# Kernel optimization log

Hardware: AMD Instinct MI355X
Metric: run time of the kernel (lower is better)

## Reference

```python
import jax, jax.numpy as jnp
import numpy as np

B, C, H, W = 8, 256, 64, 64
CI = C // 2  # inter_channels


def setup_inputs() -> dict:
    key = jax.random.key(0)
    ks = jax.random.split(key, 9)
    s_in = 1.0 / np.sqrt(C)
    s_ci = 1.0 / np.sqrt(CI)
    return {
        "x": jax.random.normal(ks[0], (B, C, H, W), dtype=jnp.float32),
        "g_w": jax.random.uniform(ks[1], (CI, C), jnp.float32, -s_in, s_in),
        "g_b": jax.random.uniform(ks[2], (CI,), jnp.float32, -s_in, s_in),
        "theta_w": jax.random.uniform(ks[3], (CI, C), jnp.float32, -s_in, s_in),
        "theta_b": jax.random.uniform(ks[4], (CI,), jnp.float32, -s_in, s_in),
        "phi_w": jax.random.uniform(ks[5], (CI, C), jnp.float32, -s_in, s_in),
        "phi_b": jax.random.uniform(ks[6], (CI,), jnp.float32, -s_in, s_in),
        "W_w": jax.random.uniform(ks[7], (C, CI), jnp.float32, -s_ci, s_ci),
        "W_b": jax.random.uniform(ks[8], (C,), jnp.float32, -s_ci, s_ci),
    }


def reference(x, g_w, g_b, theta_w, theta_b, phi_w, phi_b, W_w, W_b):
    b, c, h, w = x.shape
    xf = x.reshape(b, c, h * w)  # [B, C, N]
    # 1x1 convs == per-pixel linear maps
    g_x = jnp.einsum("oc,bcn->bon", g_w, xf) + g_b[:, None]      # [B, CI, N]
    theta_x = jnp.einsum("oc,bcn->bon", theta_w, xf) + theta_b[:, None]
    phi_x = jnp.einsum("oc,bcn->bon", phi_w, xf) + phi_b[:, None]
    # attention_map[b, i, j] = <theta[:, i], phi[:, j]>, softmax over j
    attn = jax.nn.softmax(jnp.einsum("bci,bcj->bij", theta_x, phi_x), axis=-1)
    # y[b, c, i] = sum_j g_x[b, c, j] * attn[b, i, j]
    y = jnp.einsum("bcj,bij->bci", g_x, attn)  # [B, CI, N]
    out = jnp.einsum("oc,bcn->bon", W_w, y) + W_b[:, None]  # [B, C, N]
    return out.reshape(b, c, h, w) + x
```

## Files before the change

### kernel.cpp

```cpp
#include <hip/hip_runtime.h>
#include <hip/hip_bf16.h>

#define B_  8
#define C_  256
#define CI_ 128
#define N_  4096

typedef __bf16 bf16;
typedef __attribute__((ext_vector_type(8))) __bf16 bf16x8;
typedef __attribute__((ext_vector_type(4))) __bf16 bf16x4;
typedef __attribute__((ext_vector_type(4))) float  floatx4;

static_assert(sizeof(bf16) == 2, "bf16 size");

__device__ inline floatx4 mfma16(bf16x8 a, bf16x8 b, floatx4 c) {
    return __builtin_amdgcn_mfma_f32_16x16x32_bf16(a, b, c, 0, 0, 0);
}

__device__ inline bool detect_fp32(const void* probe) {
    const unsigned short* u = (const unsigned short*)probe;
    int lane = threadIdx.x & 63;
    unsigned short w = u[lane * 2];
    int ex = (w >> 7) & 0xFF;
    bool insane = !((ex > 96 && ex < 143) || (w & 0x7FFF) == 0);
    unsigned long long b = __ballot(insane);
    return __popcll(b) > 16;
}

__device__ inline bf16x8 load8(const void* p, size_t i, bool fp32) {
    if (!fp32) return *(const bf16x8*)((const bf16*)p + i);
    const float* f = (const float*)p + i;
    floatx4 a = *(const floatx4*)(f);
    floatx4 c = *(const floatx4*)(f + 4);
    bf16x8 r;
    r[0] = (bf16)a[0]; r[1] = (bf16)a[1]; r[2] = (bf16)a[2]; r[3] = (bf16)a[3];
    r[4] = (bf16)c[0]; r[5] = (bf16)c[1]; r[6] = (bf16)c[2]; r[7] = (bf16)c[3];
    return r;
}

__device__ inline float loadv(const void* p, size_t i, bool fp32) {
    return fp32 ? ((const float*)p)[i] : (float)((const bf16*)p)[i];
}

__global__ __launch_bounds__(256) void proj_kernel(
    const void* __restrict__ x,
    const void* __restrict__ wt, const void* __restrict__ bt,
    const void* __restrict__ wp, const void* __restrict__ bp,
    const void* __restrict__ wg, const void* __restrict__ bg,
    bf16* __restrict__ T, bf16* __restrict__ P, bf16* __restrict__ G)
{
    const bool fp32 = detect_fp32(x);

    const int b    = blockIdx.y;
    const int n0   = blockIdx.x * 128;
    const int proj = blockIdx.z;

    const void* w    = (proj == 0) ? wt : (proj == 1) ? wp : wg;
    const void* bias = (proj == 0) ? bt : (proj == 1) ? bp : bg;

    __shared__ bf16 xT[128][40];

    const int t    = threadIdx.x;
    const int wid  = t >> 6;
    const int lane = t & 63;
    const int l15  = lane & 15;
    const int quad = lane >> 4;
    const int wm   = wid >> 1;
    const int wn   = wid & 1;

    floatx4 acc[4][4];
#pragma unroll
    for (int i = 0; i < 4; ++i)
#pragma unroll
        for (int j = 0; j < 4; ++j) acc[i][j] = (floatx4)0.f;

    const int cl  = t & 31;
    const int pxg = (t >> 5) * 8;

    const int obase_w = ((proj == 2) ? wm : wn) * 64;
    const int pbase_x = ((proj == 2) ? wn : wm) * 64;

    for (int k = 0; k < C_; k += 32) {
#pragma unroll
        for (int half = 0; half < 2; ++half) {
            int px = pxg + half * 64;
            bf16x8 v = load8(x, ((size_t)b * C_ + k + cl) * N_ + n0 + px, fp32);
#pragma unroll
            for (int i = 0; i < 8; ++i) xT[px + i][cl] = v[i];
        }
        __syncthreads();

        bf16x8 fw[4], fx[4];
#pragma unroll
        for (int i = 0; i < 4; ++i) {
            int o  = obase_w + i * 16 + l15;
            fw[i] = load8(w, (size_t)o * C_ + k + quad * 8, fp32);
            int px = pbase_x + i * 16 + l15;
            fx[i] = *(const bf16x8*)(&xT[px][quad * 8]);
        }
        if (proj == 2) {
#pragma unroll
            for (int mi = 0; mi < 4; ++mi)
#pragma unroll
                for (int ni = 0; ni < 4; ++ni)
                    acc[mi][ni] = mfma16(fw[mi], fx[ni], acc[mi][ni]);
        } else {
#pragma unroll
            for (int mi = 0; mi < 4; ++mi)
#pragma unroll
                for (int ni = 0; ni < 4; ++ni)
                    acc[mi][ni] = mfma16(fx[mi], fw[ni], acc[mi][ni]);
        }
        __syncthreads();
    }

    if (proj < 2) {
        bf16* out = ((proj == 0) ? T : P) + (size_t)b * N_ * CI_;
#pragma unroll
        for (int mi = 0; mi < 4; ++mi)
#pragma unroll
            for (int ni = 0; ni < 4; ++ni)
#pragma unroll
                for (int r = 0; r < 4; ++r) {
                    int px = n0 + wm * 64 + mi * 16 + quad * 4 + r;
                    int o  = wn * 64 + ni * 16 + l15;
                    out[(size_t)px * CI_ + o] =
                        (bf16)(acc[mi][ni][r] + loadv(bias, o, fp32));
                }
    } else {
        bf16* out = G + (size_t)b * CI_ * N_;
#pragma unroll
        for (int mi = 0; mi < 4; ++mi)
#pragma unroll
            for (int ni = 0; ni < 4; ++ni)
#pragma unroll
                for (int r = 0; r < 4; ++r) {
                    int o  = wm * 64 + mi * 16 + quad * 4 + r;
                    int px = n0 + wn * 64 + ni * 16 + l15;
                    out[(size_t)o * N_ + px] =
                        (bf16)(acc[mi][ni][r] + loadv(bias, o, fp32));
                }
    }
}

__global__ __launch_bounds__(512) void attn_kernel(
    const bf16* __restrict__ T,
    const bf16* __restrict__ P,
    const bf16* __restrict__ G,
    const void* __restrict__ Ww,
    const void* __restrict__ Wb,
    const void* __restrict__ x,
    void* __restrict__ out)
{
    const int bid = blockIdx.x;
    const int b   = bid & 7;
    const int i0  = (bid >> 3) * 128;

    __shared__ __align__(16) char smem[143360];

    const bool fp32 = detect_fp32(x);

    const int t    = threadIdx.x;
    const int w    = t >> 6;
    const int g    = w >> 2;
    const int wg   = w & 3;
    const int tg   = t & 255;
    const int lane = t & 63;
    const int l15  = lane & 15;
    const int quad = lane >> 4;

    bf16* Kl = (bf16*)(smem + g * 35840);
    bf16* Vt = (bf16*)(smem + g * 35840 + 17408);
    bf16* Pw = (bf16*)(smem + 71680 + w * 4608);

    const bf16* Kb = P + (size_t)b * N_ * CI_;
    const bf16* Vb = G + (size_t)b * CI_ * N_;
    const int jbase = g * 2048;

    bf16x8 qf[2][4];
#pragma unroll
    for (int rf = 0; rf < 2; ++rf) {
        const bf16* Qb = T + ((size_t)b * N_ + i0 + wg * 32 + rf * 16 + l15) * CI_;
#pragma unroll
        for (int ks = 0; ks < 4; ++ks)
            qf[rf][ks] = *(const bf16x8*)(Qb + ks * 32 + quad * 8);
    }

    floatx4 O[2][8];
#pragma unroll
    for (int rf = 0; rf < 2; ++rf)
#pragma unroll
        for (int cf = 0; cf < 8; ++cf) O[rf][cf] = (floatx4)0.f;
    float lsum[2][4];
#pragma unroll
    for (int rf = 0; rf < 2; ++rf)
#pragma unroll
        for (int r = 0; r < 4; ++r) lsum[rf][r] = 0.f;

    bf16x8 kreg[4], vreg[4];
#pragma unroll
    for (int s = 0; s < 4; ++s) {
        int id = tg + s * 256;
        kreg[s] = *(const bf16x8*)(Kb + (size_t)(jbase + (id >> 4)) * CI_ + (id & 15) * 8);
        vreg[s] = *(const bf16x8*)(Vb + (size_t)(id >> 3) * N_ + jbase + (id & 7) * 8);
    }

    for (int it = 0; it < 32; ++it) {
#pragma unroll
        for (int s = 0; s < 4; ++s) {
            int id = tg + s * 256;
            *(bf16x8*)(Kl + (id >> 4) * 136 + (id & 15) * 8) = kreg[s];
            *(bf16x8*)(Vt + (id >> 3) * 72 + (id & 7) * 8) = vreg[s];
        }
        __syncthreads();

        if (it < 31) {
            int j0n = jbase + (it + 1) * 64;
#pragma unroll
            for (int s = 0; s < 4; ++s) {
                int id = tg + s * 256;
                kreg[s] = *(const bf16x8*)(Kb + (size_t)(j0n + (id >> 4)) * CI_ + (id & 15) * 8);
                vreg[s] = *(const bf16x8*)(Vb + (size_t)(id >> 3) * N_ + j0n + (id & 7) * 8);
            }
        }

        floatx4 S[2][4];
#pragma unroll
        for (int jf = 0; jf < 4; ++jf) {
            floatx4 s0 = (floatx4)0.f, s1 = (floatx4)0.f;
#pragma unroll
            for (int ks = 0; ks < 4; ++ks) {
                bf16x8 kf = *(const bf16x8*)(Kl + (jf * 16 + l15) * 136 + ks * 32 + quad * 8);
                s0 = mfma16(qf[0][ks], kf, s0);
                s1 = mfma16(qf[1][ks], kf, s1);
            }
            S[0][jf] = s0;
            S[1][jf] = s1;
        }

#pragma unroll
        for (int rf = 0; rf < 2; ++rf)
#pragma unroll
            for (int r = 0; r < 4; ++r) {
                float p0 = __expf(S[rf][0][r]);
                float p1 = __expf(S[rf][1][r]);
                float p2 = __expf(S[rf][2][r]);
                float p3 = __expf(S[rf][3][r]);
                lsum[rf][r] += (p0 + p1) + (p2 + p3);
                int row = rf * 16 + quad * 4 + r;
                Pw[row * 72 + 0 * 16 + l15] = (bf16)p0;
                Pw[row * 72 + 1 * 16 + l15] = (bf16)p1;
                Pw[row * 72 + 2 * 16 + l15] = (bf16)p2;
                Pw[row * 72 + 3 * 16 + l15] = (bf16)p3;
            }

#pragma unroll
        for (int ks = 0; ks < 2; ++ks) {
            bf16x8 pf0 = *(const bf16x8*)(Pw + l15 * 72 + ks * 32 + quad * 8);
            bf16x8 pf1 = *(const bf16x8*)(Pw + (16 + l15) * 72 + ks * 32 + quad * 8);
#pragma unroll
            for (int cf = 0; cf < 8; ++cf) {
                bf16x8 vf = *(const bf16x8*)(Vt + (cf * 16 + l15) * 72 + ks * 32 + quad * 8);
                O[0][cf] = mfma16(pf0, vf, O[0][cf]);
                O[1][cf] = mfma16(pf1, vf, O[1][cf]);
            }
        }
        __syncthreads();
    }

    float* scrO = (float*)smem;
    float* scrL = (float*)(smem + 71680);
    bf16*  Yl   = (bf16*)(smem + 108544);
    if (g == 1) {
#pragma unroll
        for (int rf = 0; rf < 2; ++rf)
#pragma unroll
            for (int cf = 0; cf < 8; ++cf)
#pragma unroll
                for (int r = 0; r < 4; ++r)
                    scrO[(rf * 32 + cf * 4 + r) * 256 + wg * 64 + lane] = O[rf][cf][r];
#pragma unroll
        for (int rf = 0; rf < 2; ++rf)
#pragma unroll
            for (int r = 0; r < 4; ++r)
                scrL[(rf * 4 + r) * 256 + wg * 64 + lane] = lsum[rf][r];
    }
    __syncthreads();
    if (g == 0) {
#pragma unroll
        for (int rf = 0; rf < 2; ++rf)
#pragma unroll
            for (int cf = 0; cf < 8; ++cf)
#pragma unroll
                for (int r = 0; r < 4; ++r)
                    O[rf][cf][r] += scrO[(rf * 32 + cf * 4 + r) * 256 + wg * 64 + lane];

#pragma unroll
        for (int rf = 0; rf < 2; ++rf)
#pragma unroll
            for (int r = 0; r < 4; ++r) {
                float rs = lsum[rf][r] + scrL[(rf * 4 + r) * 256 + wg * 64 + lane];
                rs += __shfl_xor(rs, 1);
                rs += __shfl_xor(rs, 2);
                rs += __shfl_xor(rs, 4);
                rs += __shfl_xor(rs, 8);
                lsum[rf][r] = 1.f / rs;
            }

#pragma unroll
        for (int rf = 0; rf < 2; ++rf)
#pragma unroll
            for (int cf = 0; cf < 8; ++cf)
#pragma unroll
                for (int r = 0; r < 4; ++r) {
                    int px = wg * 32 + rf * 16 + quad * 4 + r;
                    Yl[px * 136 + cf * 16 + l15] =
                        (bf16)(O[rf][cf][r] * lsum[rf][r]);
                }
    }
    __syncthreads();

    bf16* Wl = (bf16*)smem;
#pragma unroll
    for (int p = 0; p < 16; ++p) {
        int idx = p * 2048 + t * 4;
        int o   = idx >> 7;
        int ci  = idx & 127;
        bf16x4 v;
        if (fp32) {
            floatx4 f4 = *(const floatx4*)((const float*)Ww + idx);
            v[0] = (bf16)f4[0]; v[1] = (bf16)f4[1];
            v[2] = (bf16)f4[2]; v[3] = (bf16)f4[3];
        } else {
            v = *(const bf16x4*)((const bf16*)Ww + idx);
        }
        *(bf16x4*)(&Wl[o * 136 + ci]) = v;
    }
    __syncthreads();

    {
        const int wm = w >> 1;
        const int wn = w & 1;
        floatx4 acc[4][4];
#pragma unroll
        for (int i = 0; i < 4; ++i)
#pragma unroll
            for (int j = 0; j < 4; ++j) acc[i][j] = (floatx4)0.f;

#pragma unroll
        for (int ks = 0; ks < 4; ++ks) {
            bf16x8 fa[4], fb[4];
#pragma unroll
            for (int i = 0; i < 4; ++i) {
                fa[i] = *(const bf16x8*)(&Wl[(wm * 64 + i * 16 + l15) * 136 + ks * 32 + quad * 8]);
                fb[i] = *(const bf16x8*)(&Yl[(wn * 64 + i * 16 + l15) * 136 + ks * 32 + quad * 8]);
            }
#pragma unroll
            for (int mi = 0; mi < 4; ++mi)
#pragma unroll
                for (int ni = 0; ni < 4; ++ni)
                    acc[mi][ni] = mfma16(fa[mi], fb[ni], acc[mi][ni]);
        }

#pragma unroll
        for (int mi = 0; mi < 4; ++mi)
#pragma unroll
            for (int ni = 0; ni < 4; ++ni)
#pragma unroll
                for (int r = 0; r < 4; ++r) {
                    int oo = wm * 64 + mi * 16 + quad * 4 + r;
                    int px = i0 + wn * 64 + ni * 16 + l15;
                    size_t idx = ((size_t)b * C_ + oo) * N_ + px;
                    float v = acc[mi][ni][r] + loadv(Wb, oo, fp32)
                            + loadv(x, idx, fp32);
                    if (fp32) ((float*)out)[idx] = v;
                    else      ((bf16*)out)[idx] = (bf16)v;
                }
    }
}

extern "C" void kernel_launch(void* const* d_in, const int* in_sizes, int n_in,
                              void* d_out, int out_size, void* d_ws, size_t ws_size,
                              hipStream_t stream) {
    const void* x    = d_in[0];
    const void* g_w  = d_in[1];
    const void* g_b  = d_in[2];
    const void* th_w = d_in[3];
    const void* th_b = d_in[4];
    const void* ph_w = d_in[5];
    const void* ph_b = d_in[6];
    const void* W_w  = d_in[7];
    const void* W_b  = d_in[8];

    const size_t plane = (size_t)B_ * N_ * CI_;
    bf16* T = (bf16*)d_ws;
    bf16* P = T + plane;
    bf16* G = P + plane;

    proj_kernel<<<dim3(N_ / 128, B_, 3), 256, 0, stream>>>(
        x, th_w, th_b, ph_w, ph_b, g_w, g_b, T, P, G);
    attn_kernel<<<dim3(N_ / 128 * B_), 512, 0, stream>>>(
        T, P, G, W_w, W_b, x, d_out);
}
```

Baseline: 263.5 us.

## Fuse three projections into one kernel sharing the x tile, with prefetch

```diff
diff --git a/kernel.cpp b/kernel.cpp
--- a/kernel.cpp
+++ b/kernel.cpp
@@ -42,7 +42,14 @@
     return fp32 ? ((const float*)p)[i] : (float)((const bf16*)p)[i];
 }
 
-__global__ __launch_bounds__(256) void proj_kernel(
+__device__ inline bf16x8 cvt8(floatx4 a, floatx4 b) {
+    bf16x8 r;
+    r[0] = (bf16)a[0]; r[1] = (bf16)a[1]; r[2] = (bf16)a[2]; r[3] = (bf16)a[3];
+    r[4] = (bf16)b[0]; r[5] = (bf16)b[1]; r[6] = (bf16)b[2]; r[7] = (bf16)b[3];
+    return r;
+}
+
+__global__ __launch_bounds__(512) void proj3_kernel(
     const void* __restrict__ x,
     const void* __restrict__ wt, const void* __restrict__ bt,
     const void* __restrict__ wp, const void* __restrict__ bp,
@@ -51,95 +58,127 @@
 {
     const bool fp32 = detect_fp32(x);
 
-    const int b    = blockIdx.y;
-    const int n0   = blockIdx.x * 128;
-    const int proj = blockIdx.z;
-
-    const void* w    = (proj == 0) ? wt : (proj == 1) ? wp : wg;
-    const void* bias = (proj == 0) ? bt : (proj == 1) ? bp : bg;
+    const int b  = blockIdx.y;
+    const int n0 = blockIdx.x * 128;
 
     __shared__ bf16 xT[128][40];
+    __shared__ bf16 wl[384][40];
 
     const int t    = threadIdx.x;
-    const int wid  = t >> 6;
+    const int w    = t >> 6;
     const int lane = t & 63;
     const int l15  = lane & 15;
     const int quad = lane >> 4;
-    const int wm   = wid >> 1;
-    const int wn   = wid & 1;
-
-    floatx4 acc[4][4];
-#pragma unroll
-    for (int i = 0; i < 4; ++i)
-#pragma unroll
-        for (int j = 0; j < 4; ++j) acc[i][j] = (floatx4)0.f;
-
-    const int cl  = t & 31;
-    const int pxg = (t >> 5) * 8;
-
-    const int obase_w = ((proj == 2) ? wm : wn) * 64;
-    const int pbase_x = ((proj == 2) ? wn : wm) * 64;
-
-    for (int k = 0; k < C_; k += 32) {
-#pragma unroll
-        for (int half = 0; half < 2; ++half) {
-            int px = pxg + half * 64;
-            bf16x8 v = load8(x, ((size_t)b * C_ + k + cl) * N_ + n0 + px, fp32);
-#pragma unroll
-            for (int i = 0; i < 8; ++i) xT[px + i][cl] = v[i];
+    const int wm   = w >> 1;
+    const int wn   = w & 1;
+
+    const int sc = t >> 4;
+    const int sm = t & 15;
+    const int wr = t >> 2;
+    const int wc = (t & 3) * 8;
+
+    floatx4 acc[6][4];
+#pragma unroll
+    for (int f = 0; f < 6; ++f)
+#pragma unroll
+        for (int ni = 0; ni < 4; ++ni) acc[f][ni] = (floatx4)0.f;
+
+    floatx4 pxa, pxb; bf16x8 pxh;
+    floatx4 pwa[3], pwb[3]; bf16x8 pwh[3];
+
+    auto issue = [&](int k) {
+        size_t xo = ((size_t)b * C_ + k + sc) * N_ + n0 + sm * 8;
+        if (fp32) {
+            const float* fx_ = (const float*)x + xo;
+            pxa = *(const floatx4*)fx_;
+            pxb = *(const floatx4*)(fx_ + 4);
+        } else {
+            pxh = *(const bf16x8*)((const bf16*)x + xo);
+        }
+#pragma unroll
+        for (int p = 0; p < 3; ++p) {
+            const void* ws = (p == 0) ? wt : (p == 1) ? wp : wg;
+            size_t wo = (size_t)wr * C_ + k + wc;
+            if (fp32) {
+                const float* fw_ = (const float*)ws + wo;
+                pwa[p] = *(const floatx4*)fw_;
+                pwb[p] = *(const floatx4*)(fw_ + 4);
+            } else {
+                pwh[p] = *(const bf16x8*)((const bf16*)ws + wo);
+            }
+        }
+    };
+
+    issue(0);
+
+    for (int ks = 0; ks < 8; ++ks) {
+        {
+            bf16x8 xv = fp32 ? cvt8(pxa, pxb) : pxh;
+            int colx = ((((sc >> 3) + sm) & 3) << 3) + (sc & 7);
+#pragma unroll
+            for (int i = 0; i < 8; ++i) xT[sm * 8 + i][colx] = xv[i];
+#pragma unroll
+            for (int p = 0; p < 3; ++p) {
+                bf16x8 wv = fp32 ? cvt8(pwa[p], pwb[p]) : pwh[p];
+                *(bf16x8*)(&wl[p * 128 + wr][wc]) = wv;
+            }
         }
         __syncthreads();
 
-        bf16x8 fw[4], fx[4];
-#pragma unroll
-        for (int i = 0; i < 4; ++i) {
-            int o  = obase_w + i * 16 + l15;
-            fw[i] = load8(w, (size_t)o * C_ + k + quad * 8, fp32);
-            int px = pbase_x + i * 16 + l15;
-            fx[i] = *(const bf16x8*)(&xT[px][quad * 8]);
-        }
-        if (proj == 2) {
-#pragma unroll
-            for (int mi = 0; mi < 4; ++mi)
-#pragma unroll
-                for (int ni = 0; ni < 4; ++ni)
-                    acc[mi][ni] = mfma16(fw[mi], fx[ni], acc[mi][ni]);
+        if (ks < 7) issue((ks + 1) * 32);
+
+        bf16x8 fxr[4], fwr[6];
+#pragma unroll
+        for (int ni = 0; ni < 4; ++ni) {
+            int px = wn * 64 + ni * 16 + l15;
+            int ch = (quad + (px >> 3)) & 3;
+            fxr[ni] = *(const bf16x8*)(&xT[px][ch * 8]);
+        }
+#pragma unroll
+        for (int f = 0; f < 6; ++f)
+            fwr[f] = *(const bf16x8*)(&wl[f * 64 + wm * 16 + l15][quad * 8]);
+
+#pragma unroll
+        for (int f = 0; f < 4; ++f)
+#pragma unroll
+            for (int ni = 0; ni < 4; ++ni)
+                acc[f][ni] = mfma16(fxr[ni], fwr[f], acc[f][ni]);
+#pragma unroll
+        for (int f = 4; f < 6; ++f)
+#pragma unroll
+            for (int ni = 0; ni < 4; ++ni)
+                acc[f][ni] = mfma16(fwr[f], fxr[ni], acc[f][ni]);
+
+        __syncthreads();
+    }
+
+#pragma unroll
+    for (int f = 0; f < 6; ++f) {
+        const void* bsel = (f < 2) ? bt : (f < 4) ? bp : bg;
+        if (f < 4) {
+            bf16* outp = ((f < 2) ? T : P) + (size_t)b * N_ * CI_;
+            int o = (f & 1) * 64 + wm * 16 + l15;
+            float bv = loadv(bsel, o, fp32);
+#pragma unroll
+            for (int ni = 0; ni < 4; ++ni)
+#pragma unroll
+                for (int r = 0; r < 4; ++r) {
+                    int px = n0 + wn * 64 + ni * 16 + quad * 4 + r;
+                    outp[(size_t)px * CI_ + o] = (bf16)(acc[f][ni][r] + bv);
+                }
         } else {
-#pragma unroll
-            for (int mi = 0; mi < 4; ++mi)
-#pragma unroll
-                for (int ni = 0; ni < 4; ++ni)
-                    acc[mi][ni] = mfma16(fx[mi], fw[ni], acc[mi][ni]);
-        }
-        __syncthreads();
-    }
-
-    if (proj < 2) {
-        bf16* out = ((proj == 0) ? T : P) + (size_t)b * N_ * CI_;
-#pragma unroll
-        for (int mi = 0; mi < 4; ++mi)
-#pragma unroll
-            for (int ni = 0; ni < 4; ++ni)
-#pragma unroll
-                for (int r = 0; r < 4; ++r) {
-                    int px = n0 + wm * 64 + mi * 16 + quad * 4 + r;
-                    int o  = wn * 64 + ni * 16 + l15;
-                    out[(size_t)px * CI_ + o] =
-                        (bf16)(acc[mi][ni][r] + loadv(bias, o, fp32));
+            bf16* outp = G + (size_t)b * CI_ * N_;
+#pragma unroll
+            for (int r = 0; r < 4; ++r) {
+                int o = (f & 1) * 64 + wm * 16 + quad * 4 + r;
+                float bv = loadv(bsel, o, fp32);
+#pragma unroll
+                for (int ni = 0; ni < 4; ++ni) {
+                    int px = n0 + wn * 64 + ni * 16 + l15;
+                    outp[(size_t)o * N_ + px] = (bf16)(acc[f][ni][r] + bv);
                 }
-    } else {
-        bf16* out = G + (size_t)b * CI_ * N_;
-#pragma unroll
-        for (int mi = 0; mi < 4; ++mi)
-#pragma unroll
-            for (int ni = 0; ni < 4; ++ni)
-#pragma unroll
-                for (int r = 0; r < 4; ++r) {
-                    int o  = wm * 64 + mi * 16 + quad * 4 + r;
-                    int px = n0 + wn * 64 + ni * 16 + l15;
-                    out[(size_t)o * N_ + px] =
-                        (bf16)(acc[mi][ni][r] + loadv(bias, o, fp32));
-                }
+            }
+        }
     }
 }
 
@@ -397,7 +436,7 @@
     bf16* P = T + plane;
     bf16* G = P + plane;
 
-    proj_kernel<<<dim3(N_ / 128, B_, 3), 256, 0, stream>>>(
+    proj3_kernel<<<dim3(N_ / 128, B_), 512, 0, stream>>>(
         x, th_w, th_b, ph_w, ph_b, g_w, g_b, T, P, G);
     attn_kernel<<<dim3(N_ / 128 * B_), 512, 0, stream>>>(
         T, P, G, W_w, W_b, x, d_out);
```

Result: faster. 214.6 us (-18.6%).
